# Performance work log

Hardware: AMD Instinct MI355X
Metric: run time of the kernel (lower is better)

The kernel has to match this reference:

```python
import jax, jax.numpy as jnp
import numpy as np
from jax import lax

D_MODEL = 60
D_INNER = 120   # expand=2
D_STATE = 16
D_CONV = 4
DT_RANK = 4     # ceil(60/16)
DEPTH = 2
BATCH = 2
H_IMG = 128
W_IMG = 128
L_SEQ = H_IMG * W_IMG


def setup_inputs() -> dict:
    key = jax.random.key(0)
    ks = jax.random.split(key, 12)
    s = 0.02
    x = jax.random.normal(ks[0], (BATCH, L_SEQ, D_MODEL), jnp.float32)
    ln_w = jnp.ones((DEPTH, D_MODEL), jnp.float32)
    ln_b = jnp.zeros((DEPTH, D_MODEL), jnp.float32)
    in_proj_w = jax.random.normal(ks[1], (DEPTH, 2 * D_INNER, D_MODEL), jnp.float32) * s
    conv_w = jax.random.normal(ks[2], (DEPTH, D_INNER, D_CONV), jnp.float32) * s
    conv_b = jnp.zeros((DEPTH, D_INNER), jnp.float32)
    x_proj_w = jax.random.normal(ks[3], (DEPTH, DT_RANK + 2 * D_STATE, D_INNER), jnp.float32) * s
    dt_proj_w = jax.random.normal(ks[4], (DEPTH, D_INNER, DT_RANK), jnp.float32) * s
    dt_proj_b = jnp.full((DEPTH, D_INNER), -4.0, jnp.float32)  # softplus^-1 of small dt
    A_log = jnp.broadcast_to(
        jnp.log(jnp.arange(1, D_STATE + 1, dtype=jnp.float32))[None, None, :],
        (DEPTH, D_INNER, D_STATE)).copy()
    D_skip = jnp.ones((DEPTH, D_INNER), jnp.float32)
    out_proj_w = jax.random.normal(ks[5], (DEPTH, D_MODEL, D_INNER), jnp.float32) * s
    conv2d_w = jax.random.normal(ks[6], (D_MODEL, D_MODEL, 3, 3), jnp.float32) * s
    conv2d_b = jnp.zeros((D_MODEL,), jnp.float32)
    return {"x": x, "ln_w": ln_w, "ln_b": ln_b, "in_proj_w": in_proj_w,
            "conv_w": conv_w, "conv_b": conv_b, "x_proj_w": x_proj_w,
            "dt_proj_w": dt_proj_w, "dt_proj_b": dt_proj_b, "A_log": A_log,
            "D": D_skip, "out_proj_w": out_proj_w,
            "conv2d_w": conv2d_w, "conv2d_b": conv2d_b,
            "H": H_IMG, "W": W_IMG}


def _layernorm(x, w, b, eps=1e-5):
    mu = jnp.mean(x, axis=-1, keepdims=True)
    var = jnp.mean(jnp.square(x - mu), axis=-1, keepdims=True)
    return (x - mu) * lax.rsqrt(var + eps) * w + b


def _selective_scan(dA, dBx, C):
    # dA, dBx: [B, L, D_INNER, D_STATE]; C: [B, L, D_STATE]
    def step(h, inp):
        dA_t, dBx_t, c_t = inp
        h = dA_t * h + dBx_t                       # [B, D_INNER, D_STATE]
        y = jnp.einsum('bdn,bn->bd', h, c_t)
        return h, y
    h0 = jnp.zeros(dA.shape[:1] + dA.shape[2:], dA.dtype)
    _, ys = lax.scan(step, h0,
                     (dA.transpose(1, 0, 2, 3), dBx.transpose(1, 0, 2, 3),
                      C.transpose(1, 0, 2)))
    return ys.transpose(1, 0, 2)                    # [B, L, D_INNER]


def _mamba(x, in_w, cw, cb, xp_w, dtw, dtb, A_log, D_skip, out_w):
    # x: [B, L, D_MODEL]
    xz = jnp.einsum('bld,ed->ble', x, in_w)         # [B, L, 2*D_INNER]
    xin, z = jnp.split(xz, 2, axis=-1)
    # causal depthwise conv1d over L
    xc = xin.transpose(0, 2, 1)                     # [B, D_INNER, L]
    xc = jnp.pad(xc, ((0, 0), (0, 0), (D_CONV - 1, 0)))
    xc = lax.conv_general_dilated(xc, cw[:, None, :], (1,), 'VALID',
                                  dimension_numbers=('NCH', 'OIH', 'NCH'),
                                  feature_group_count=D_INNER)
    xc = jax.nn.silu(xc + cb[None, :, None]).transpose(0, 2, 1)  # [B, L, D_INNER]
    xdb = jnp.einsum('bld,ed->ble', xc, xp_w)       # [B, L, DT_RANK + 2*D_STATE]
    dt = xdb[..., :DT_RANK]
    Bm = xdb[..., DT_RANK:DT_RANK + D_STATE]
    Cm = xdb[..., DT_RANK + D_STATE:]
    delta = jax.nn.softplus(jnp.einsum('blr,dr->bld', dt, dtw) + dtb)  # [B, L, D_INNER]
    A = -jnp.exp(A_log)                              # [D_INNER, D_STATE]
    dA = jnp.exp(delta[..., None] * A[None, None])   # [B, L, D_INNER, D_STATE]
    dBx = delta[..., None] * Bm[:, :, None, :] * xc[..., None]
    y = _selective_scan(dA, dBx, Cm) + D_skip * xc
    y = y * jax.nn.silu(z)
    return jnp.einsum('ble,de->bld', y, out_w)       # [B, L, D_MODEL]


def reference(x, ln_w, ln_b, in_proj_w, conv_w, conv_b, x_proj_w,
              dt_proj_w, dt_proj_b, A_log, D, out_proj_w,
              conv2d_w, conv2d_b, H, W):
    h = x
    for i in range(DEPTH):
        hn = _layernorm(h, ln_w[i], ln_b[i])
        h = _mamba(hn, in_proj_w[i], conv_w[i], conv_b[i], x_proj_w[i],
                   dt_proj_w[i], dt_proj_b[i], A_log[i], D[i], out_proj_w[i])
    # patch_unembed -> 3x3 conv -> patch_embed, residual add (RMMB)
    b = h.shape[0]
    img = h.transpose(0, 2, 1).reshape(b, D_MODEL, H, W)
    img = lax.conv_general_dilated(img, conv2d_w, (1, 1), 'SAME',
                                   dimension_numbers=('NCHW', 'OIHW', 'NCHW'))
    img = img + conv2d_b[None, :, None, None]
    h = img.reshape(b, D_MODEL, H * W).transpose(0, 2, 1)
    return h + x
```

## Files before the change

kernel.cpp:

```cpp
#include <hip/hip_runtime.h>
#include <math.h>

#define BATCH 2
#define LSEQ 16384
#define DM 60
#define DI 120
#define NCH 512
#define TCH 32
#define HH 128
#define WW 128

typedef __attribute__((ext_vector_type(8))) short bhalf8;
typedef __attribute__((ext_vector_type(4))) short short4v;
typedef __attribute__((ext_vector_type(4))) float f32x4;

__device__ __forceinline__ float sigmoidf_(float x){ return __builtin_amdgcn_rcpf(1.0f + __expf(-x)); }
__device__ __forceinline__ float siluf_(float x){ return x * sigmoidf_(x); }
__device__ __forceinline__ float softplusf_(float x){ return (x > 20.0f) ? x : __logf(1.0f + __expf(x)); }
__device__ __forceinline__ short f2b(float f){
  union{float f; unsigned u;} v; v.f = f;
  unsigned r = (v.u + 0x7fffu + ((v.u >> 16) & 1u)) >> 16;
  return (short)r;
}
__device__ __forceinline__ float b2f(short s){
  union{float f; unsigned u;} v; v.u = ((unsigned)(unsigned short)s) << 16; return v.f;
}

__device__ __forceinline__ void powers8(float r, float* p){
  p[0] = r;
  #pragma unroll
  for (int n = 1; n < 8; n++) p[n] = p[(n-1)>>1] * p[n>>1];
}

__global__ __launch_bounds__(256) void k_pack(
    const float* __restrict__ ipw, const float* __restrict__ xpw,
    const float* __restrict__ opw, const float* __restrict__ c2w,
    const float* __restrict__ lnw, const float* __restrict__ lnb,
    short* __restrict__ pk, float* __restrict__ c01, short* __restrict__ wB)
{
  int i = blockIdx.x*256 + threadIdx.x;
  if (i < 2*240*64){
    int l = i / (240*64);
    int rem = i % (240*64);
    int n = rem / 64, k = rem % 64;
    float v = (k < 60) ? ipw[(size_t)l*14400 + n*60 + k] * lnw[l*60 + k] : 0.f;
    pk[i] = f2b(v);
  } else if (i < 30720 + 2*48*128){
    int j = i - 30720;
    int l = j / (48*128);
    int rem = j % (48*128);
    int n = rem / 128, k = rem % 128;
    float v = (n < 36 && k < 120) ? xpw[(size_t)l*36*120 + n*120 + k] : 0.f;
    pk[i] = f2b(v);
  } else if (i < 43008 + 480){
    int j = i - 43008;
    int l = j / 240, n = j % 240;
    float c1 = 0.f, c0 = 0.f;
    for (int k = 0; k < 60; k++){
      float w = ipw[(size_t)l*14400 + n*60 + k];
      c1 += lnw[l*60+k] * w;
      c0 += lnb[l*60+k] * w;
    }
    c01[(l*240 + n)*2 + 0] = c1;
    c01[(l*240 + n)*2 + 1] = c0;
  } else if (i < 43488 + 2*64*128){
    int j = i - 43488;
    int l = j / 8192;
    int rem = j % 8192;
    int n = rem / 128, k = rem % 128;
    float v = (n < 60 && k < 120) ? opw[(size_t)l*7200 + n*120 + k] : 0.f;
    pk[43008 + j] = f2b(v);
  } else if (i < 59872 + 9*64*64){
    int j = i - 59872;
    int ci = j & 63, co = (j >> 6) & 63, tap = j >> 12;
    float v = 0.f;
    if (co < 60 && ci < 60) v = c2w[((size_t)co*60 + ci)*9 + tap];
    wB[j] = f2b(v);
  }
}

__global__ __launch_bounds__(512) void k_lnxp(
    const float* __restrict__ srcf, const short* __restrict__ srcb,
    const short* __restrict__ ipB,
    const float* __restrict__ c01,
    const float* __restrict__ cw, const float* __restrict__ cb,
    const short* __restrict__ xpB,
    const float* __restrict__ dtw, const float* __restrict__ dtb,
    const float* __restrict__ A_log,
    short* __restrict__ zs, short* __restrict__ xcg,
    short* __restrict__ delta, short* __restrict__ BCg,
    float* __restrict__ ap, float* __restrict__ he)
{
  __shared__ __align__(16) char smem[65056];
  short* XB   = (short*)smem;
  short* xcB  = (short*)smem;
  short* xinB = (short*)(smem + 8704);
  float* delLf= (float*)(smem + 8704);
  float* xcf  = (float*)(smem + 24064);
  float* BLf  = (float*)(smem + 39424);
  short* BCL  = (short*)(smem + 41472);
  float* stats= (float*)(smem + 43520);
  float* dtsh = (float*)(smem + 43904);
  float* cwL  = (float*)(smem + 44416);
  float* Wd5T = (float*)(smem + 46336);
  float* cbL  = (float*)(smem + 48256);
  float* bdL  = (float*)(smem + 48736);
  float* A20L = (float*)(smem + 49216);
  float* rL   = (float*)(smem + 49696);
  const int tid = threadIdx.x;
  const int wave = tid >> 6, lane = tid & 63;
  const int m = lane & 15, quad = lane >> 4;
  const int row0 = blockIdx.x * 32;
  const int seq0 = (row0 / LSEQ) * LSEQ;
  if (tid < 480){ cwL[tid] = cw[tid]; Wd5T[(tid & 3)*120 + (tid >> 2)] = dtw[tid]; }
  if (tid < 120){
    cbL[tid] = cb[tid]; bdL[tid] = dtb[tid];
    A20L[tid] = -__expf(A_log[tid*16]) * 1.44269504f;
  }
  for (int i = tid; i < 48*16; i += 512){
    int r = i >> 4, g = i & 15;
    int grow = row0 - 3 + r;
    short4v o = {0,0,0,0};
    if (g < 15 && r < 35 && grow >= seq0){
      if (srcb){
        o = *(const short4v*)&srcb[(size_t)grow*60 + g*4];
      } else {
        float4 f = *(const float4*)&srcf[(size_t)grow*60 + g*4];
        o.x = f2b(f.x); o.y = f2b(f.y); o.z = f2b(f.z); o.w = f2b(f.w);
      }
    }
    *(short4v*)&XB[r*72 + g*4] = o;
  }
  __syncthreads();
  {
    const int sub = lane >> 4;
    const int li  = lane & 15;
    #pragma unroll
    for (int it = 0; it < 2; it++){
      int r = it*32 + wave*4 + sub;
      if (r < 48){
        short4v x4 = *(const short4v*)&XB[r*72 + li*4];
        float f0 = b2f(x4.x), f1 = b2f(x4.y), f2 = b2f(x4.z), f3 = b2f(x4.w);
        float sx = (f0 + f1) + (f2 + f3);
        float sq = (f0*f0 + f1*f1) + (f2*f2 + f3*f3);
        #pragma unroll
        for (int off = 1; off < 16; off <<= 1){
          sx += __shfl_xor(sx, off);
          sq += __shfl_xor(sq, off);
        }
        if (li == 0){
          float mu = sx * (1.0f/60.0f);
          float var = fmaxf(sq * (1.0f/60.0f) - mu*mu, 0.f);
          stats[r*2 + 0] = mu;
          stats[r*2 + 1] = rsqrtf(var + 1e-5f);
        }
      }
    }
  }
  __syncthreads();
  for (int t = wave; t < 45; t += 8){
    int mtile = t / 15, ntile = t % 15;
    f32x4 acc = {0.f,0.f,0.f,0.f};
    #pragma unroll
    for (int ks = 0; ks < 2; ks++){
      bhalf8 a = *(const bhalf8*)&XB[(mtile*16 + m)*72 + ks*32 + quad*8];
      bhalf8 b = *(const bhalf8*)&ipB[(ntile*16 + m)*64 + ks*32 + quad*8];
      acc = __builtin_amdgcn_mfma_f32_16x16x32_bf16(a, b, acc, 0, 0, 0);
    }
    int n = ntile*16 + m;
    float2 cc = *(const float2*)&c01[n*2];
    float c1v = cc.x, c0v = cc.y;
    #pragma unroll
    for (int reg = 0; reg < 4; reg++){
      int r = mtile*16 + quad*4 + reg;
      int grow = row0 - 3 + r;
      bool valid = (r < 35) && (grow >= seq0);
      float mu = stats[r*2], rs = stats[r*2+1];
      float val = rs*(acc[reg] - mu*c1v) + c0v;
      if (!valid) val = 0.f;
      if (n < 120){
        xinB[r*136 + n] = f2b(val);
      } else if (r >= 3 && r < 35){
        zs[(size_t)(row0 - 3 + r)*120 + (n - 120)] = f2b(siluf_(val));
      }
    }
  }
  __syncthreads();
  for (int i = tid; i < 960; i += 512){
    int r = i/30, c4 = (i%30)*4;
    float4 cbv = *(const float4*)&cbL[c4];
    float4 w0 = *(const float4*)&cwL[(c4+0)*4];
    float4 w1 = *(const float4*)&cwL[(c4+1)*4];
    float4 w2 = *(const float4*)&cwL[(c4+2)*4];
    float4 w3 = *(const float4*)&cwL[(c4+3)*4];
    short4v x0 = *(const short4v*)&xinB[(r+0)*136 + c4];
    short4v x1 = *(const short4v*)&xinB[(r+1)*136 + c4];
    short4v x2 = *(const short4v*)&xinB[(r+2)*136 + c4];
    short4v x3 = *(const short4v*)&xinB[(r+3)*136 + c4];
    float a0 = cbv.x + w0.x*b2f(x0.x) + w0.y*b2f(x1.x) + w0.z*b2f(x2.x) + w0.w*b2f(x3.x);
    float a1 = cbv.y + w1.x*b2f(x0.y) + w1.y*b2f(x1.y) + w1.z*b2f(x2.y) + w1.w*b2f(x3.y);
    float a2 = cbv.z + w2.x*b2f(x0.z) + w2.y*b2f(x1.z) + w2.z*b2f(x2.z) + w2.w*b2f(x3.z);
    float a3 = cbv.w + w3.x*b2f(x0.w) + w3.y*b2f(x1.w) + w3.z*b2f(x2.w) + w3.w*b2f(x3.w);
    a0 = siluf_(a0); a1 = siluf_(a1); a2 = siluf_(a2); a3 = siluf_(a3);
    float4 fo; fo.x = a0; fo.y = a1; fo.z = a2; fo.w = a3;
    *(float4*)&xcf[r*120 + c4] = fo;
    short4v o;
    o.x = f2b(a0); o.y = f2b(a1); o.z = f2b(a2); o.w = f2b(a3);
    *(short4v*)&xcB[r*136 + c4] = o;
  }
  for (int i = tid; i < 32*8; i += 512)
    xcB[(i >> 3)*136 + 120 + (i & 7)] = 0;
  __syncthreads();
  for (int t = wave; t < 6; t += 8){
    int mtile = t / 3, ntile = t % 3;
    f32x4 acc = {0.f,0.f,0.f,0.f};
    #pragma unroll
    for (int ks = 0; ks < 4; ks++){
      bhalf8 a = *(const bhalf8*)&xcB[(mtile*16 + m)*136 + ks*32 + quad*8];
      bhalf8 b = *(const bhalf8*)&xpB[(ntile*16 + m)*128 + ks*32 + quad*8];
      acc = __builtin_amdgcn_mfma_f32_16x16x32_bf16(a, b, acc, 0, 0, 0);
    }
    int n = ntile*16 + m;
    #pragma unroll
    for (int reg = 0; reg < 4; reg++){
      int r = mtile*16 + quad*4 + reg;
      float val = acc[reg];
      if (n < 4)        dtsh[r*4 + n] = val;
      else if (n < 36){
        BCL[r*32 + (n - 4)] = f2b(val);
        if (n < 20) BLf[r*16 + (n - 4)] = val;
      }
    }
  }
  __syncthreads();
  for (int i = tid; i < 960; i += 512){
    int row = i/30, c4 = (i%30)*4;
    float4 t4 = *(const float4*)&dtsh[row*4];
    float4 w0 = *(const float4*)&Wd5T[0*120 + c4];
    float4 w1 = *(const float4*)&Wd5T[1*120 + c4];
    float4 w2 = *(const float4*)&Wd5T[2*120 + c4];
    float4 w3 = *(const float4*)&Wd5T[3*120 + c4];
    float4 bb = *(const float4*)&bdL[c4];
    float4 dd;
    dd.x = softplusf_(bb.x + t4.x*w0.x + t4.y*w1.x + t4.z*w2.x + t4.w*w3.x);
    dd.y = softplusf_(bb.y + t4.x*w0.y + t4.y*w1.y + t4.z*w2.y + t4.w*w3.y);
    dd.z = softplusf_(bb.z + t4.x*w0.z + t4.y*w1.z + t4.z*w2.z + t4.w*w3.z);
    dd.w = softplusf_(bb.w + t4.x*w0.w + t4.y*w1.w + t4.z*w2.w + t4.w*w3.w);
    *(float4*)&delLf[row*120 + c4] = dd;
    float4 aa = *(const float4*)&A20L[c4];
    float4 rr4;
    rr4.x = exp2f(dd.x * aa.x);
    rr4.y = exp2f(dd.y * aa.y);
    rr4.z = exp2f(dd.z * aa.z);
    rr4.w = exp2f(dd.w * aa.w);
    *(float4*)&rL[row*120 + c4] = rr4;
    short4v o;
    o.x = f2b(dd.x); o.y = f2b(dd.y); o.z = f2b(dd.z); o.w = f2b(dd.w);
    *(short4v*)&delta[(size_t)(row0 + row)*120 + c4] = o;
  }
  __syncthreads();
  for (int i = tid; i < 960; i += 512){
    int r = i/30, off = (i%30)*4;
    *(short4v*)&xcg[(size_t)(row0 + r)*120 + off] = *(const short4v*)&xcB[r*136 + off];
  }
  for (int i = tid; i < 256; i += 512)
    *(short4v*)&BCg[(size_t)row0*32 + i*4] = *(const short4v*)&BCL[i*4];
  if (tid < 480){
    const int d = tid >> 2, q = tid & 3, n0 = q << 2;
    const int b = row0 / LSEQ;
    const int cglob = (row0 % LSEQ) >> 5;
    float A2[4], h[4];
    const float A20 = A20L[d];
    #pragma unroll
    for (int n = 0; n < 4; n++){
      A2[n] = -__expf(A_log[d*16 + n0 + n]) * 1.44269504f;
      h[n] = 0.f;
    }
    bool fastp = true;
    #pragma unroll
    for (int n = 0; n < 4; n++)
      fastp = fastp && (fabsf(A2[n] - (n0+n+1)*A20) <= 1e-4f*fabsf(A2[n]));
    int fp = fastp ? 1 : 0;
    fp &= __shfl_xor(fp, 1);
    fp &= __shfl_xor(fp, 2);
    const int sh1 = q & 1, sh2 = q & 2;
    int base = (cglob*BATCH + b)*(DI*16) + d*16 + n0;
    if (fp){
      float P = 1.f;
      for (int t = 0; t < 32; t += 2){
        float d1 = delLf[t*120 + d],     d2 = delLf[(t+1)*120 + d];
        float x1 = xcf[t*120 + d],       x2 = xcf[(t+1)*120 + d];
        float dx1 = d1*x1, dx2 = d2*x2;
        float r2s = rL[(t+1)*120 + d];
        float rr  = rL[t*120 + d] * r2s;
        P *= rr;
        float c1 = rr*rr, c2 = c1*rr, c3 = c1*c1;
        float sc = sh1 ? c3 : 1.0f; if (sh2) sc *= c3*c3;
        float p1 = r2s*r2s, p2 = p1*r2s, p3 = p1*p1;
        float s2 = sh1 ? p3 : 1.0f; if (sh2) s2 *= p3*p3;
        float4 b1 = *(const float4*)&BLf[t*16 + n0];
        float4 b2 = *(const float4*)&BLf[(t+1)*16 + n0];
        float ad0 = (s2*r2s)*dx1*b1.x + dx2*b2.x;
        float ad1 = (s2*p1 )*dx1*b1.y + dx2*b2.y;
        float ad2 = (s2*p2 )*dx1*b1.z + dx2*b2.z;
        float ad3 = (s2*p3 )*dx1*b1.w + dx2*b2.w;
        h[0] = (sc*rr)*h[0] + ad0;
        h[1] = (sc*c1)*h[1] + ad1;
        h[2] = (sc*c2)*h[2] + ad2;
        h[3] = (sc*c3)*h[3] + ad3;
      }
      float P1 = P*P;
      float P2 = P1*P, P3 = P1*P1;
      float sP = sh1 ? P3 : 1.0f;
      if (sh2) sP *= P3*P3;
      float apv[4] = {sP*P, sP*P1, sP*P2, sP*P3};
      *(float4*)&ap[base] = *(float4*)&apv[0];
      *(float4*)&he[base] = *(float4*)&h[0];
    } else {
      float apv[4] = {1.f,1.f,1.f,1.f};
      for (int t = 0; t < 32; t++){
        float del = delLf[t*120 + d];
        float dx = del * xcf[t*120 + d];
        #pragma unroll
        for (int n = 0; n < 4; n++){
          float dA = exp2f(del * A2[n]);
          apv[n] *= dA;
          h[n] = dA*h[n] + dx*BLf[t*16 + n0 + n];
        }
      }
      *(float4*)&ap[base] = *(float4*)&apv[0];
      *(float4*)&he[base] = *(float4*)&h[0];
    }
  }
}

__global__ __launch_bounds__(256) void k_scan2(float* __restrict__ ap, const float* __restrict__ he)
{
  __shared__ float aggA[16*17];
  __shared__ float aggB[16*17];
  const int tid = threadIdx.x;
  const int n = tid & 15, j = tid >> 4;
  const int sbase = blockIdx.x*16 + n;
  const int stride = BATCH*DI*16;
  {
    float A = 1.f, B = 0.f;
    int idx = (j*32)*stride + sbase;
    #pragma unroll 4
    for (int k = 0; k < 32; k++){
      float a = ap[idx], h = he[idx];
      B = a*B + h;
      A *= a;
      idx += stride;
    }
    aggA[n*17 + j] = A;
    aggB[n*17 + j] = B;
  }
  __syncthreads();
  if (tid < 16){
    float B = 0.f;
    #pragma unroll
    for (int jj = 0; jj < 16; jj++){
      float Af = aggA[tid*17 + jj];
      float Bf = aggB[tid*17 + jj];
      aggB[tid*17 + jj] = B;
      B = Af*B + Bf;
    }
  }
  __syncthreads();
  {
    float H = aggB[n*17 + j];
    int idx = (j*32)*stride + sbase;
    #pragma unroll 4
    for (int k = 0; k < 32; k++){
      float a = ap[idx], h = he[idx];
      ap[idx] = H;
      H = a*H + h;
      idx += stride;
    }
  }
}

__global__ __launch_bounds__(256) void k_scan3o(
    const short* __restrict__ delta, const short* __restrict__ xc,
    const short* __restrict__ BCg, const short* __restrict__ zs,
    const float* __restrict__ h0, const float* __restrict__ A_log,
    const float* __restrict__ Dsk, const short* __restrict__ opB,
    short* __restrict__ hout)
{
  __shared__ float BCl[TCH*32];
  __shared__ __align__(16) short yL[TCH*136];
  __shared__ __align__(16) short dL[TCH*120];
  __shared__ __align__(16) short xL[TCH*120];
  __shared__ __align__(16) short zL[TCH*120];
  const int tid = threadIdx.x;
  const int wave = tid >> 6, lane = tid & 63;
  const int m = lane & 15, quad = lane >> 4;
  const int c = blockIdx.x % NCH, b = blockIdx.x / NCH;
  const size_t rowbase = (size_t)b*LSEQ + (size_t)c*TCH;
  for (int i = tid; i < 960; i += 256)
    *(short4v*)&dL[i*4] = *(const short4v*)&delta[rowbase*DI + i*4];
  for (int i = tid; i < 960; i += 256)
    *(short4v*)&xL[i*4] = *(const short4v*)&xc[rowbase*DI + i*4];
  for (int i = tid; i < 960; i += 256)
    *(short4v*)&zL[i*4] = *(const short4v*)&zs[rowbase*DI + i*4];
  for (int i = tid; i < TCH*8; i += 256){
    short4v v = *(const short4v*)&BCg[rowbase*32 + i*4];
    float4 f; f.x = b2f(v.x); f.y = b2f(v.y); f.z = b2f(v.z); f.w = b2f(v.w);
    *(float4*)&BCl[i*4] = f;
  }
  for (int i = tid; i < TCH*4; i += 256){
    short4v z = {0,0,0,0};
    *(short4v*)&yL[(i >> 2)*136 + 120 + (i & 3)*4] = z;
  }
  __syncthreads();
  if (tid < 240){
    const int d = tid >> 1, half = tid & 1, n0 = half << 3;
    float A2[8], h[8];
    const int base = (c*BATCH + b)*(DI*16) + d*16 + n0;
    const float A20 = -__expf(A_log[d*16]) * 1.44269504f;
    #pragma unroll
    for (int n = 0; n < 8; n++){
      A2[n] = -__expf(A_log[d*16 + n0 + n]) * 1.44269504f;
      h[n] = h0[base + n];
    }
    bool fastp = true;
    #pragma unroll
    for (int n = 0; n < 8; n++)
      fastp = fastp && (fabsf(A2[n] - (n0+n+1)*A20) <= 1e-4f*fabsf(A2[n]));
    int fp = fastp ? 1 : 0;
    fp &= __shfl_xor(fp, 1);
    const float Dv = Dsk[d];
    if (fp){
      for (int t = 0; t < TCH; t++){
        float del = b2f(dL[t*120 + d]);
        float xcv = b2f(xL[t*120 + d]);
        float zv  = b2f(zL[t*120 + d]);
        float dx = del * xcv;
        float r = exp2f(del * A20);
        float p8[8]; powers8(r, p8);
        float s = half ? p8[7] : 1.0f;
        float4 b0 = *(const float4*)&BCl[t*32 + n0];
        float4 b1 = *(const float4*)&BCl[t*32 + n0 + 4];
        h[0] = (s*p8[0])*h[0] + dx*b0.x;  h[1] = (s*p8[1])*h[1] + dx*b0.y;
        h[2] = (s*p8[2])*h[2] + dx*b0.z;  h[3] = (s*p8[3])*h[3] + dx*b0.w;
        h[4] = (s*p8[4])*h[4] + dx*b1.x;  h[5] = (s*p8[5])*h[5] + dx*b1.y;
        h[6] = (s*p8[6])*h[6] + dx*b1.z;  h[7] = (s*p8[7])*h[7] + dx*b1.w;
        float4 c0 = *(const float4*)&BCl[t*32 + 16 + n0];
        float4 c1 = *(const float4*)&BCl[t*32 + 20 + n0];
        float acc = h[0]*c0.x + h[1]*c0.y + h[2]*c0.z + h[3]*c0.w
                  + h[4]*c1.x + h[5]*c1.y + h[6]*c1.z + h[7]*c1.w;
        acc += __shfl_xor(acc, 1);
        if (!half) yL[t*136 + d] = f2b((acc + Dv*xcv) * zv);
      }
    } else {
      for (int t = 0; t < TCH; t++){
        float del = b2f(dL[t*120 + d]);
        float xcv = b2f(xL[t*120 + d]);
        float zv  = b2f(zL[t*120 + d]);
        float dx = del * xcv;
        float acc = 0.f;
        #pragma unroll
        for (int n = 0; n < 8; n++){
          float dA = exp2f(del * A2[n]);
          h[n] = dA*h[n] + dx*BCl[t*32 + n0 + n];
          acc += h[n]*BCl[t*32 + 16 + n0 + n];
        }
        acc += __shfl_xor(acc, 1);
        if (!half) yL[t*136 + d] = f2b((acc + Dv*xcv) * zv);
      }
    }
  }
  __syncthreads();
  for (int t = wave; t < 8; t += 4){
    const int mtile = t >> 2, ntile = t & 3;
    f32x4 acc = {0.f,0.f,0.f,0.f};
    #pragma unroll
    for (int ks = 0; ks < 4; ks++){
      bhalf8 a  = *(const bhalf8*)&yL[(mtile*16 + m)*136 + ks*32 + quad*8];
      bhalf8 bb = *(const bhalf8*)&opB[(ntile*16 + m)*128 + ks*32 + quad*8];
      acc = __builtin_amdgcn_mfma_f32_16x16x32_bf16(a, bb, acc, 0, 0, 0);
    }
    const int n = ntile*16 + m;
    if (n < 60){
      #pragma unroll
      for (int reg = 0; reg < 4; reg++){
        int r = mtile*16 + quad*4 + reg;
        hout[(rowbase + r)*60 + n] = f2b(acc[reg]);
      }
    }
  }
}

__global__ __launch_bounds__(256) void k_conv2d(
    const short* __restrict__ hin, const short* __restrict__ wB,
    const float* __restrict__ cb, const float* __restrict__ xres,
    float* __restrict__ out)
{
  __shared__ short tile[3*66*72];
  const int tid = threadIdx.x;
  const int blk = blockIdx.x;
  const int xhalf = blk & 1;
  const int yy = (blk >> 1) & 127;
  const int b = blk >> 8;
  const int x0 = xhalf*64;
  for (int i = tid; i < 3*66*18; i += 256){
    int g = i % 18;
    int xx = (i / 18) % 66;
    int row = i / (18*66);
    int gy = yy - 1 + row, gx = x0 - 1 + xx;
    short4v v = {0,0,0,0};
    if (g < 15 && gy >= 0 && gy < HH && gx >= 0 && gx < WW)
      v = *(const short4v*)&hin[((size_t)b*LSEQ + gy*WW + gx)*60 + g*4];
    *(short4v*)&tile[(row*66 + xx)*72 + g*4] = v;
  }
  __syncthreads();
  const int wave = tid >> 6, lane = tid & 63;
  const int m = lane & 15, quad = lane >> 4;
  f32x4 acc0 = {0.f,0.f,0.f,0.f}, acc1 = {0.f,0.f,0.f,0.f};
  f32x4 acc2 = {0.f,0.f,0.f,0.f}, acc3 = {0.f,0.f,0.f,0.f};
  #pragma unroll
  for (int tap = 0; tap < 9; tap++){
    const int ky = tap/3, kx = tap%3;
    const short* arow = &tile[(ky*66 + wave*16 + m + kx)*72];
    const short* brow = wB + tap*4096;
    #pragma unroll
    for (int kh = 0; kh < 2; kh++){
      const int k0 = kh*32 + quad*8;
      bhalf8 a = *(const bhalf8*)(arow + k0);
      bhalf8 b0 = *(const bhalf8*)(brow + (0*16 + m)*64 + k0);
      bhalf8 b1 = *(const bhalf8*)(brow + (1*16 + m)*64 + k0);
      bhalf8 b2 = *(const bhalf8*)(brow + (2*16 + m)*64 + k0);
      bhalf8 b3 = *(const bhalf8*)(brow + (3*16 + m)*64 + k0);
      acc0 = __builtin_amdgcn_mfma_f32_16x16x32_bf16(a, b0, acc0, 0, 0, 0);
      acc1 = __builtin_amdgcn_mfma_f32_16x16x32_bf16(a, b1, acc1, 0, 0, 0);
      acc2 = __builtin_amdgcn_mfma_f32_16x16x32_bf16(a, b2, acc2, 0, 0, 0);
      acc3 = __builtin_amdgcn_mfma_f32_16x16x32_bf16(a, b3, acc3, 0, 0, 0);
    }
  }
  const size_t rowb = (size_t)b*LSEQ + yy*WW + x0;
  f32x4 accs[4] = {acc0, acc1, acc2, acc3};
  #pragma unroll
  for (int nt = 0; nt < 4; nt++){
    int co = nt*16 + m;
    if (co < 60){
      float bias = cb[co];
      #pragma unroll
      for (int reg = 0; reg < 4; reg++){
        int px = wave*16 + quad*4 + reg;
        size_t o = (rowb + px)*60 + co;
        out[o] = accs[nt][reg] + bias + xres[o];
      }
    }
  }
}

extern "C" void kernel_launch(void* const* d_in, const int* in_sizes, int n_in,
                              void* d_out, int out_size, void* d_ws, size_t ws_size,
                              hipStream_t stream)
{
  const float* x      = (const float*)d_in[0];
  const float* ln_w   = (const float*)d_in[1];
  const float* ln_b   = (const float*)d_in[2];
  const float* ipw    = (const float*)d_in[3];
  const float* cw     = (const float*)d_in[4];
  const float* cb1    = (const float*)d_in[5];
  const float* xpw    = (const float*)d_in[6];
  const float* dtw    = (const float*)d_in[7];
  const float* dtb    = (const float*)d_in[8];
  const float* A_log  = (const float*)d_in[9];
  const float* Dsk    = (const float*)d_in[10];
  const float* opw    = (const float*)d_in[11];
  const float* c2w    = (const float*)d_in[12];
  const float* c2b    = (const float*)d_in[13];
  float* out = (float*)d_out;

  char* ws = (char*)d_ws;
  size_t off = 0;
  short* zsb   = (short*)(ws + off); off += (size_t)BATCH*LSEQ*DI*2;
  short* xcb   = (short*)(ws + off); off += (size_t)BATCH*LSEQ*DI*2;
  short* dlt   = (short*)(ws + off); off += (size_t)BATCH*LSEQ*DI*2;
  short* BCg   = (short*)(ws + off); off += (size_t)BATCH*LSEQ*32*2;
  float* apb   = (float*)(ws + off); off += (size_t)NCH*BATCH*DI*16*4;
  float* heb   = (float*)(ws + off); off += (size_t)NCH*BATCH*DI*16*4;
  short* hcur  = (short*)(ws + off); off += (size_t)BATCH*LSEQ*DM*2;
  short* wBb   = (short*)(ws + off); off += (size_t)9*64*64*2;
  short* pkb   = (short*)(ws + off); off += (size_t)(2*240*64 + 2*48*128 + 2*64*128)*2;
  float* c01b  = (float*)(ws + off); off += (size_t)2*240*2*4;

  const int rows = BATCH*LSEQ;
  k_pack<<<(59872 + 9*64*64 + 255)/256, 256, 0, stream>>>(ipw, xpw, opw, c2w, ln_w, ln_b, pkb, c01b, wBb);
  for (int layer = 0; layer < 2; layer++){
    const float* srcf = (layer == 0) ? x : nullptr;
    const short* srcb = (layer == 0) ? nullptr : hcur;
    k_lnxp<<<rows/32, 512, 0, stream>>>(srcf, srcb,
                                        pkb + (size_t)layer*240*64,
                                        c01b + (size_t)layer*240*2,
                                        cw + layer*DI*4, cb1 + layer*DI,
                                        pkb + 30720 + (size_t)layer*48*128,
                                        dtw + (size_t)layer*DI*4, dtb + layer*DI,
                                        A_log + (size_t)layer*DI*16,
                                        zsb, xcb, dlt, BCg, apb, heb);
    k_scan2<<<BATCH*DI, 256, 0, stream>>>(apb, heb);
    k_scan3o<<<BATCH*NCH, 256, 0, stream>>>(dlt, xcb, BCg, zsb, apb, A_log + (size_t)layer*DI*16,
                                            Dsk + layer*DI, pkb + 43008 + (size_t)layer*8192, hcur);
  }
  k_conv2d<<<BATCH*HH*2, 256, 0, stream>>>(hcur, wBb, c2b, x, out);
}
```

Measured before the change: 254.2 us.

## Split scan3o chunks into half-chunks using mid-chunk state snapshots from lnxp

```diff
diff --git a/kernel.cpp b/kernel.cpp
--- a/kernel.cpp
+++ b/kernel.cpp
@@ -89,7 +89,8 @@
     const float* __restrict__ A_log,
     short* __restrict__ zs, short* __restrict__ xcg,
     short* __restrict__ delta, short* __restrict__ BCg,
-    float* __restrict__ ap, float* __restrict__ he)
+    float* __restrict__ ap, float* __restrict__ he,
+    float* __restrict__ ah, float* __restrict__ bh)
 {
   __shared__ __align__(16) char smem[65056];
   short* XB   = (short*)smem;
@@ -288,6 +289,13 @@
     if (fp){
       float P = 1.f;
       for (int t = 0; t < 32; t += 2){
+        if (t == 16){
+          float q1 = P*P, q2 = q1*P, q3 = q1*q1;
+          float sQ = sh1 ? q3 : 1.0f; if (sh2) sQ *= q3*q3;
+          float am[4] = {sQ*P, sQ*q1, sQ*q2, sQ*q3};
+          *(float4*)&ah[base] = *(float4*)&am[0];
+          *(float4*)&bh[base] = *(float4*)&h[0];
+        }
         float d1 = delLf[t*120 + d],     d2 = delLf[(t+1)*120 + d];
         float x1 = xcf[t*120 + d],       x2 = xcf[(t+1)*120 + d];
         float dx1 = d1*x1, dx2 = d2*x2;
@@ -319,6 +327,10 @@
     } else {
       float apv[4] = {1.f,1.f,1.f,1.f};
       for (int t = 0; t < 32; t++){
+        if (t == 16){
+          *(float4*)&ah[base] = *(float4*)&apv[0];
+          *(float4*)&bh[base] = *(float4*)&h[0];
+        }
         float del = delLf[t*120 + d];
         float dx = del * xcf[t*120 + d];
         #pragma unroll
@@ -383,32 +395,36 @@
 __global__ __launch_bounds__(256) void k_scan3o(
     const short* __restrict__ delta, const short* __restrict__ xc,
     const short* __restrict__ BCg, const short* __restrict__ zs,
-    const float* __restrict__ h0, const float* __restrict__ A_log,
+    const float* __restrict__ h0, const float* __restrict__ Ah,
+    const float* __restrict__ Bh, const float* __restrict__ A_log,
     const float* __restrict__ Dsk, const short* __restrict__ opB,
     short* __restrict__ hout)
 {
-  __shared__ float BCl[TCH*32];
-  __shared__ __align__(16) short yL[TCH*136];
-  __shared__ __align__(16) short dL[TCH*120];
-  __shared__ __align__(16) short xL[TCH*120];
-  __shared__ __align__(16) short zL[TCH*120];
+  __shared__ float BCl[16*32];
+  __shared__ __align__(16) short yL[16*136];
+  __shared__ __align__(16) short dL[16*120];
+  __shared__ __align__(16) short xL[16*120];
+  __shared__ __align__(16) short zL[16*120];
   const int tid = threadIdx.x;
   const int wave = tid >> 6, lane = tid & 63;
   const int m = lane & 15, quad = lane >> 4;
-  const int c = blockIdx.x % NCH, b = blockIdx.x / NCH;
-  const size_t rowbase = (size_t)b*LSEQ + (size_t)c*TCH;
-  for (int i = tid; i < 960; i += 256)
+  const int blk = blockIdx.x;
+  const int hc = blk & 1;
+  const int c  = (blk >> 1) % NCH;
+  const int b  = blk >> 10;
+  const size_t rowbase = (size_t)b*LSEQ + (size_t)c*TCH + (size_t)hc*16;
+  for (int i = tid; i < 480; i += 256)
     *(short4v*)&dL[i*4] = *(const short4v*)&delta[rowbase*DI + i*4];
-  for (int i = tid; i < 960; i += 256)
+  for (int i = tid; i < 480; i += 256)
     *(short4v*)&xL[i*4] = *(const short4v*)&xc[rowbase*DI + i*4];
-  for (int i = tid; i < 960; i += 256)
+  for (int i = tid; i < 480; i += 256)
     *(short4v*)&zL[i*4] = *(const short4v*)&zs[rowbase*DI + i*4];
-  for (int i = tid; i < TCH*8; i += 256){
+  for (int i = tid; i < 128; i += 256){
     short4v v = *(const short4v*)&BCg[rowbase*32 + i*4];
     float4 f; f.x = b2f(v.x); f.y = b2f(v.y); f.z = b2f(v.z); f.w = b2f(v.w);
     *(float4*)&BCl[i*4] = f;
   }
-  for (int i = tid; i < TCH*4; i += 256){
+  for (int i = tid; i < 64; i += 256){
     short4v z = {0,0,0,0};
     *(short4v*)&yL[(i >> 2)*136 + 120 + (i & 3)*4] = z;
   }
@@ -418,11 +434,24 @@
     float A2[8], h[8];
     const int base = (c*BATCH + b)*(DI*16) + d*16 + n0;
     const float A20 = -__expf(A_log[d*16]) * 1.44269504f;
-    #pragma unroll
-    for (int n = 0; n < 8; n++){
+    float4 h0a = *(const float4*)&h0[base];
+    float4 h0b = *(const float4*)&h0[base + 4];
+    if (hc){
+      float4 Aa = *(const float4*)&Ah[base];
+      float4 Ab = *(const float4*)&Ah[base + 4];
+      float4 Ba = *(const float4*)&Bh[base];
+      float4 Bb = *(const float4*)&Bh[base + 4];
+      h[0] = Aa.x*h0a.x + Ba.x;  h[1] = Aa.y*h0a.y + Ba.y;
+      h[2] = Aa.z*h0a.z + Ba.z;  h[3] = Aa.w*h0a.w + Ba.w;
+      h[4] = Ab.x*h0b.x + Bb.x;  h[5] = Ab.y*h0b.y + Bb.y;
+      h[6] = Ab.z*h0b.z + Bb.z;  h[7] = Ab.w*h0b.w + Bb.w;
+    } else {
+      h[0] = h0a.x; h[1] = h0a.y; h[2] = h0a.z; h[3] = h0a.w;
+      h[4] = h0b.x; h[5] = h0b.y; h[6] = h0b.z; h[7] = h0b.w;
+    }
+    #pragma unroll
+    for (int n = 0; n < 8; n++)
       A2[n] = -__expf(A_log[d*16 + n0 + n]) * 1.44269504f;
-      h[n] = h0[base + n];
-    }
     bool fastp = true;
     #pragma unroll
     for (int n = 0; n < 8; n++)
@@ -431,7 +460,7 @@
     fp &= __shfl_xor(fp, 1);
     const float Dv = Dsk[d];
     if (fp){
-      for (int t = 0; t < TCH; t++){
+      for (int t = 0; t < 16; t++){
         float del = b2f(dL[t*120 + d]);
         float xcv = b2f(xL[t*120 + d]);
         float zv  = b2f(zL[t*120 + d]);
@@ -453,7 +482,7 @@
         if (!half) yL[t*136 + d] = f2b((acc + Dv*xcv) * zv);
       }
     } else {
-      for (int t = 0; t < TCH; t++){
+      for (int t = 0; t < 16; t++){
         float del = b2f(dL[t*120 + d]);
         float xcv = b2f(xL[t*120 + d]);
         float zv  = b2f(zL[t*120 + d]);
@@ -471,12 +500,12 @@
     }
   }
   __syncthreads();
-  for (int t = wave; t < 8; t += 4){
-    const int mtile = t >> 2, ntile = t & 3;
+  for (int t = wave; t < 4; t += 4){
+    const int ntile = t;
     f32x4 acc = {0.f,0.f,0.f,0.f};
     #pragma unroll
     for (int ks = 0; ks < 4; ks++){
-      bhalf8 a  = *(const bhalf8*)&yL[(mtile*16 + m)*136 + ks*32 + quad*8];
+      bhalf8 a  = *(const bhalf8*)&yL[m*136 + ks*32 + quad*8];
       bhalf8 bb = *(const bhalf8*)&opB[(ntile*16 + m)*128 + ks*32 + quad*8];
       acc = __builtin_amdgcn_mfma_f32_16x16x32_bf16(a, bb, acc, 0, 0, 0);
     }
@@ -484,7 +513,7 @@
     if (n < 60){
       #pragma unroll
       for (int reg = 0; reg < 4; reg++){
-        int r = mtile*16 + quad*4 + reg;
+        int r = quad*4 + reg;
         hout[(rowbase + r)*60 + n] = f2b(acc[reg]);
       }
     }
@@ -582,6 +611,8 @@
   short* BCg   = (short*)(ws + off); off += (size_t)BATCH*LSEQ*32*2;
   float* apb   = (float*)(ws + off); off += (size_t)NCH*BATCH*DI*16*4;
   float* heb   = (float*)(ws + off); off += (size_t)NCH*BATCH*DI*16*4;
+  float* ahb   = (float*)(ws + off); off += (size_t)NCH*BATCH*DI*16*4;
+  float* bhb   = (float*)(ws + off); off += (size_t)NCH*BATCH*DI*16*4;
   short* hcur  = (short*)(ws + off); off += (size_t)BATCH*LSEQ*DM*2;
   short* wBb   = (short*)(ws + off); off += (size_t)9*64*64*2;
   short* pkb   = (short*)(ws + off); off += (size_t)(2*240*64 + 2*48*128 + 2*64*128)*2;
@@ -599,10 +630,11 @@
                                         pkb + 30720 + (size_t)layer*48*128,
                                         dtw + (size_t)layer*DI*4, dtb + layer*DI,
                                         A_log + (size_t)layer*DI*16,
-                                        zsb, xcb, dlt, BCg, apb, heb);
+                                        zsb, xcb, dlt, BCg, apb, heb, ahb, bhb);
     k_scan2<<<BATCH*DI, 256, 0, stream>>>(apb, heb);
-    k_scan3o<<<BATCH*NCH, 256, 0, stream>>>(dlt, xcb, BCg, zsb, apb, A_log + (size_t)layer*DI*16,
-                                            Dsk + layer*DI, pkb + 43008 + (size_t)layer*8192, hcur);
+    k_scan3o<<<BATCH*NCH*2, 256, 0, stream>>>(dlt, xcb, BCg, zsb, apb, ahb, bhb,
+                                              A_log + (size_t)layer*DI*16,
+                                              Dsk + layer*DI, pkb + 43008 + (size_t)layer*8192, hcur);
   }
   k_conv2d<<<BATCH*HH*2, 256, 0, stream>>>(hcur, wBb, c2b, x, out);
 }
```

After: 257.1 us. About the same (+1.1%).
